# Performance work log

Hardware: AMD Instinct MI355X
Metric: run time of the kernel (lower is better)

## Reference

```python
import jax, jax.numpy as jnp
import numpy as np

B, L, D, W = 4, 256, 256, 8  # batch, seq_len, d_model, context_window
NS_EPS = 1e-7


def setup_inputs() -> dict:
    key = jax.random.key(0)
    ks = jax.random.split(key, 12)
    f = lambda k, s: jax.random.normal(k, s, dtype=jnp.float32)
    sD = 1.0 / np.sqrt(D)
    return {
        "x": f(ks[0], (B, L, D)),
        "k_aligned": jnp.tanh(f(ks[1], (B, L, D))),  # QKProjectionLayer applies tanh upstream
        "v": f(ks[2], (B, L, D)),
        "M_prev": f(ks[3], (B, D, D)) * 0.01,
        "S_prev": jnp.zeros((B, D, D), jnp.float32),
        # polynomial feature coeffs: phi(k) = c1*k + c2*k^2 (degree 2, dim-preserving)
        "poly_coeffs": jnp.stack([jnp.ones((D,), jnp.float32), 0.1 * jnp.ones((D,), jnp.float32)])
        + 0.01 * f(ks[4], (2, D)),
        "alpha_W": f(ks[5], (D, D)) * sD, "alpha_b": jnp.zeros((D,), jnp.float32),
        "eta_W": f(ks[6], (D, D)) * sD, "eta_b": jnp.zeros((D,), jnp.float32),
        "theta_W": f(ks[7], (D, D)) * sD, "theta_b": jnp.zeros((D,), jnp.float32),
        "gamma_W": f(ks[8], (D,)) * sD, "gamma_b": jnp.zeros((1,), jnp.float32),
        "out_W": f(ks[9], (D, D)) * sD, "out_b": jnp.zeros((D,), jnp.float32),
    }


def _newton_schulz_1(S):
    # NS_K with K=1: X <- 1.5*X - 0.5*X X^T X after Frobenius normalization
    norm = jnp.sqrt(jnp.sum(S * S, axis=(-2, -1), keepdims=True)) + NS_EPS
    X = S / norm
    return 1.5 * X - 0.5 * jnp.einsum('bij,bkj,bkl->bil', X, X, X)


def reference(x, k_aligned, v, M_prev, S_prev, poly_coeffs,
              alpha_W, alpha_b, eta_W, eta_b, theta_W, theta_b,
              gamma_W, gamma_b, out_W, out_b):
    Bn, Ln, Dn = x.shape
    # polynomial feature layer (dim-preserving, degree 2)
    k_phi = poly_coeffs[0] * k_aligned + poly_coeffs[1] * k_aligned ** 2  # [B,L,D]
    # per-token gates (precomputed, pure linear+sigmoid)
    alpha = jax.nn.sigmoid(x @ alpha_W.T + alpha_b)          # [B,L,D]
    eta = jax.nn.sigmoid(x @ eta_W.T + eta_b) * 0.1          # [B,L,D]
    theta = jax.nn.sigmoid(x @ theta_W.T + theta_b)          # [B,L,D]
    gamma = jax.nn.sigmoid(jnp.einsum('bld,d->bl', x, gamma_W) + gamma_b[0])  # [B,L]
    c_arr = jnp.minimum(jnp.arange(Ln) + 1, W).astype(x.dtype)  # actual window length per step

    to_t = lambda a: jnp.moveaxis(a, 1, 0)  # [B,L,...] -> [L,B,...]
    xs = (to_t(k_phi), to_t(v), to_t(gamma), to_t(alpha), to_t(eta), to_t(theta), c_arr)

    buf_k = jnp.zeros((Bn, W, Dn), x.dtype)  # sliding window of phi(k); zero pads contribute 0
    buf_v = jnp.zeros((Bn, W, Dn), x.dtype)
    buf_g = jnp.zeros((Bn, W), x.dtype)

    def step(carry, xt):
        M, S, bk, bv, bg = carry
        k_t, v_t, g_t, a_t, e_t, th_t, c_t = xt
        bk = jnp.concatenate([bk[:, 1:], k_t[:, None]], axis=1)
        bv = jnp.concatenate([bv[:, 1:], v_t[:, None]], axis=1)
        bg = jnp.concatenate([bg[:, 1:], g_t[:, None]], axis=1)
        # Omega gradient: sum_i gamma_i * (M phi(k_i) - v_i) outer phi(k_i) / c
        pred = jnp.einsum('bde,bwe->bwd', M, bk)
        err = pred - bv
        grad = jnp.einsum('bw,bwd,bwe->bde', bg, err, bk) / c_t
        S = th_t[..., None] * S + grad
        S_ortho = _newton_schulz_1(S)
        M = a_t[..., None] * M - e_t[..., None] * S_ortho
        y = jnp.einsum('bde,be->bd', M, k_t)
        return (M, S, bk, bv, bg), y

    (M, S, _, _, _), ys = jax.lax.scan(step, (M_prev, S_prev, buf_k, buf_v, buf_g), xs)
    output = jnp.moveaxis(ys, 0, 1) @ out_W.T + out_b  # out_proj per token
    return (output, M, S)
```

## Files before the change

### kernel.cpp

```cpp
#include <hip/hip_runtime.h>

#define Bn 4
#define Ln 256
#define Dn 256
#define Wn 8
#define NBLK 64
#define BLD (Bn*Ln*Dn)
#define BDD (Bn*Dn*Dn)

typedef float  floatx4 __attribute__((ext_vector_type(4)));
typedef short  short8  __attribute__((ext_vector_type(8)));

__device__ __forceinline__ float ldc(const float* p) {
    return __hip_atomic_load(p, __ATOMIC_RELAXED, __HIP_MEMORY_SCOPE_AGENT);
}
__device__ __forceinline__ void stc(float* p, float v) {
    __hip_atomic_store(p, v, __ATOMIC_RELAXED, __HIP_MEMORY_SCOPE_AGENT);
}
__device__ __forceinline__ void stc4(float* p, floatx4 v) {
    asm volatile("global_store_dwordx4 %0, %1, off sc0 sc1" :: "v"(p), "v"(v) : "memory");
}
__device__ __forceinline__ void ldc1x4(float& a, float& b, float& c, float& d,
    const float* p0, const float* p1, const float* p2, const float* p3)
{
    asm volatile(
        "global_load_dword %0, %4, off sc0 sc1\n\t"
        "global_load_dword %1, %5, off sc0 sc1\n\t"
        "global_load_dword %2, %6, off sc0 sc1\n\t"
        "global_load_dword %3, %7, off sc0 sc1\n\t"
        "s_waitcnt vmcnt(0)"
        : "=&v"(a), "=&v"(b), "=&v"(c), "=&v"(d)
        : "v"(p0), "v"(p1), "v"(p2), "v"(p3)
        : "memory");
}
__device__ __forceinline__ void ldc4x12s(
    floatx4& r0, floatx4& r1, floatx4& r2, floatx4& r3,
    floatx4& r4, floatx4& r5, floatx4& r6, floatx4& r7,
    floatx4& r8, floatx4& r9, floatx4& r10, floatx4& r11, float& sc,
    const float* p0, const float* p1, const float* p2, const float* p3,
    const float* p4, const float* p5, const float* p6, const float* p7,
    const float* p8, const float* p9, const float* p10, const float* p11,
    const float* ps)
{
    asm volatile(
        "global_load_dwordx4 %0, %13, off sc0 sc1\n\t"
        "global_load_dwordx4 %1, %14, off sc0 sc1\n\t"
        "global_load_dwordx4 %2, %15, off sc0 sc1\n\t"
        "global_load_dwordx4 %3, %16, off sc0 sc1\n\t"
        "global_load_dwordx4 %4, %17, off sc0 sc1\n\t"
        "global_load_dwordx4 %5, %18, off sc0 sc1\n\t"
        "global_load_dwordx4 %6, %19, off sc0 sc1\n\t"
        "global_load_dwordx4 %7, %20, off sc0 sc1\n\t"
        "global_load_dwordx4 %8, %21, off sc0 sc1\n\t"
        "global_load_dwordx4 %9, %22, off sc0 sc1\n\t"
        "global_load_dwordx4 %10, %23, off sc0 sc1\n\t"
        "global_load_dwordx4 %11, %24, off sc0 sc1\n\t"
        "global_load_dword %12, %25, off sc0 sc1\n\t"
        "s_waitcnt vmcnt(0)"
        : "=&v"(r0), "=&v"(r1), "=&v"(r2), "=&v"(r3),
          "=&v"(r4), "=&v"(r5), "=&v"(r6), "=&v"(r7),
          "=&v"(r8), "=&v"(r9), "=&v"(r10), "=&v"(r11), "=&v"(sc)
        : "v"(p0), "v"(p1), "v"(p2), "v"(p3), "v"(p4), "v"(p5),
          "v"(p6), "v"(p7), "v"(p8), "v"(p9), "v"(p10), "v"(p11), "v"(ps)
        : "memory");
}

__device__ __forceinline__ unsigned f2bf(float x) {
    unsigned u = __float_as_uint(x);
    return (u + 0x7FFFu + ((u >> 16) & 1u)) >> 16;
}
__device__ __forceinline__ unsigned long long packbf4(floatx4 v) {
    unsigned lo = f2bf(v[0]) | (f2bf(v[1]) << 16);
    unsigned hi = f2bf(v[2]) | (f2bf(v[3]) << 16);
    return (unsigned long long)lo | ((unsigned long long)hi << 32);
}
union BF8 { short8 s8; unsigned long long u[2]; };

__device__ __forceinline__ void grid_sync_b(unsigned* bflags, int rem, unsigned k)
// ... 110 lines not shown

__global__ __launch_bounds__(256) void ysum_kernel(float* __restrict__ ysp)
{
    int gidx = blockIdx.x * 256 + threadIdx.x;
    float4 a = ((float4*)ysp)[gidx];
    float4 b = ((float4*)ysp)[65536 + gidx];
    float4 c = ((float4*)ysp)[131072 + gidx];
    float4 d = ((float4*)ysp)[196608 + gidx];
    a.x += b.x + c.x + d.x;
    a.y += b.y + c.y + d.y;
    a.z += b.z + c.z + d.z;
    a.w += b.w + c.w + d.w;
    ((float4*)ysp)[gidx] = a;
}

#define OFF_ST    0
#define OFF_UV    8448
#define OFF_AV    10496
#define OFF_CV    12544
#define OFF_TH    14592
#define OFF_KT    14848
#define OFF_KL    15104
#define OFF_NRM   15168
#define OFF_WSUM  15184
#define OFF_US    15200
#define OFF_KWA   15328
#define OFF_KW2   17408
#define OFF_SL    19456
#define SMEM_FLOATS 23616

__global__ void __launch_bounds__(256, 1) scan_kernel(
    const float* __restrict__ kphi, const float* __restrict__ vin,
    const float* __restrict__ gammaB, const float* __restrict__ alphaB,
    const float* __restrict__ etaB, const float* __restrict__ thetaB,
    const float* __restrict__ Kall,
    const float* __restrict__ Mprev, const float* __restrict__ Sprev,
    unsigned short* __restrict__ STg,
    float* __restrict__ u_buf, float* __restrict__ a_buf,
    float* __restrict__ errp_g, float* __restrict__ normp,
    float* __restrict__ ysp, unsigned* __restrict__ flags,
    float* __restrict__ outM, float* __restrict__ outS)
{
    __shared__ float smem[SMEM_FLOATS];
    char*  STb  = (char*)(smem + OFF_ST);
    float* uvp  = smem + OFF_UV;
    float* avp  = smem + OFF_AV;
    float* cvp  = smem + OFF_CV;
    float* thv  = smem + OFF_TH;
    float* kT   = smem + OFF_KT;
    float* Kl   = smem + OFF_KL;
    float* nrml = smem + OFF_NRM;
    float* wsum = smem + OFF_WSUM;
    float* usl  = smem + OFF_US;
    float* kWA  = smem + OFF_KWA;
    float* kW2  = smem + OFF_KW2;
    float* Sl   = smem + OFF_SL;

    const int wg = blockIdx.x, tid = threadIdx.x;
    const int b   = wg >> 4;
    const int rem = wg & 15;
    const int s   = rem & 3;
    const int i0 = (rem >> 2) * 64, l0 = (rem & 3) * 64;
    const int d0 = rem << 4;
    const int wid = tid >> 6, lane = tid & 63;
    const int lme = lane & 15, hi = lane >> 4;
    const int ibr = i0 + wid * 16 + (hi << 2);
    const int r  = tid >> 4, m = tid & 15;
    unsigned* bflags = flags + b * 512;
    unsigned kbar = 0;

    floatx4 S_reg[4];
    float   M_reg[16];
    floatx4 T_reg[16];

    {
#pragma unroll
        for (int cq = 0; cq < 4; ++cq)
            S_reg[cq] = *(const floatx4*)&Sprev[(size_t)(b*256 + d0 + r)*256 + m*4 + 64*cq];
#pragma unroll
        for (int lt = 0; lt < 4; ++lt)
#pragma unroll
            for (int g = 0; g < 4; ++g)
                M_reg[lt*4+g] = Mprev[(size_t)(b*256 + ibr + g)*256 + l0 + lt*16 + lme];

        float* scratch = smem;
        for (int g4 = 0; g4 < 4; ++g4) {
            floatx4 acc[4];
#pragma unroll
            for (int lt = 0; lt < 4; ++lt) acc[lt] = (floatx4){0.f,0.f,0.f,0.f};
#pragma unroll
            for (int kc = 0; kc < 8; ++kc) {
                int kb2 = kc*32 + hi*8;
                floatx4 a0 = *(const floatx4*)&Sprev[(size_t)(b*256 + i0 + wid*16 + lme)*256 + kb2];
// ... 8 lines not shown
                    acc[lt] = __builtin_amdgcn_mfma_f32_16x16x32_bf16(ua.s8, ub.s8, acc[lt], 0,0,0);
                }
            }
#pragma unroll
            for (int lt = 0; lt < 4; ++lt)
#pragma unroll
                for (int g = 0; g < 4; ++g)
                    scratch[(wid*16 + (hi<<2) + g)*260 + g4*64 + lt*16 + lme] = acc[lt][g];
        }
        __syncthreads();
#pragma unroll
        for (int kc = 0; kc < 8; ++kc) {
            T_reg[kc*2+0] = *(floatx4*)&scratch[(wid*16 + lme)*260 + kc*32 + hi*8];
            T_reg[kc*2+1] = *(floatx4*)&scratch[(wid*16 + lme)*260 + kc*32 + hi*8 + 4];
        }
#pragma unroll
        for (int q = 0; q < 2; ++q) {
            int w = q*4 + (tid >> 6);
            int c4 = (tid & 63) << 2;
            floatx4 kv = {0.f,0.f,0.f,0.f};
            if (w == 7) kv = *(const floatx4*)&kphi[(size_t)(b*Ln)*Dn + c4];
            *(floatx4*)&kW2[w*256 + c4] = kv;
        }
        __syncthreads();
#pragma unroll
        for (int w = 0; w < 8; ++w) {
            float pd[4] = {0.f,0.f,0.f,0.f};
#pragma unroll
            for (int lt = 0; lt < 4; ++lt) {
                float kv2 = kW2[w*256 + l0 + lt*16 + lme];
#pragma unroll
                for (int g = 0; g < 4; ++g) pd[g] += M_reg[lt*4+g] * kv2;
            }
#pragma unroll
            for (int g = 0; g < 4; ++g) {
                pd[g] += __shfl_xor(pd[g], 1); pd[g] += __shfl_xor(pd[g], 2);
                pd[g] += __shfl_xor(pd[g], 4); pd[g] += __shfl_xor(pd[g], 8);
            }
            if (lme == 0)
#pragma unroll
                for (int g = 0; g < 4; ++g)
                    stc(&errp_g[(size_t)((s*2 + 0)*4 + b)*2048 + w*256 + ibr + g], pd[g]);
        }
    }
    grid_sync_b(bflags, rem, ++kbar);

    for (int t = 0; t < Ln; ++t) {
        const int cwin = (t + 1 < Wn) ? (t + 1) : Wn;
        const float invc = 1.f / (float)cwin;

        {
            float e0_ = 0.f, e1_ = 0.f, e2_ = 0.f, e3_ = 0.f;
            int w_a = 0, rr_a = 0;
            const int p = t & 1;
            if (tid < 128) {
                w_a = tid >> 4; rr_a = tid & 15;
                ldc1x4(e0_, e1_, e2_, e3_,
                    &errp_g[(size_t)((0*2 + p)*4 + b)*2048 + w_a*256 + d0 + rr_a],
                    &errp_g[(size_t)((1*2 + p)*4 + b)*2048 + w_a*256 + d0 + rr_a],
                    &errp_g[(size_t)((2*2 + p)*4 + b)*2048 + w_a*256 + d0 + rr_a],
                    &errp_g[(size_t)((3*2 + p)*4 + b)*2048 + w_a*256 + d0 + rr_a]);
                float ep = e0_ + e1_ + e2_ + e3_;
                int tok = t - 7 + w_a;
                float uu = 0.f;
                if (tok >= 0)
                    uu = gammaB[b*Ln + tok] * invc *
                         (ep - vin[(size_t)(b*Ln + tok)*Dn + d0 + rr_a]);
                usl[w_a*16 + rr_a] = uu;
                stc(&u_buf[(size_t)(b*8 + w_a)*256 + d0 + rr_a], uu);
            } else {
                int idx = tid - 128;
                int w = idx >> 4, seg = idx & 15;
                int tk = t - 7 + w;
#pragma unroll
                for (int q = 0; q < 4; ++q) {
                    floatx4 kv = {0.f,0.f,0.f,0.f};
                    if (tk >= 0)
                        kv = *(const floatx4*)&kphi[(size_t)(b*Ln + tk)*Dn + seg*16 + q*4];
                    *(floatx4*)&kWA[w*260 + seg*16 + q*4] = kv;
                }
            }
            __syncthreads();

            {
                float qw[8] = {0,0,0,0,0,0,0,0};
#pragma unroll
                for (int cq = 0; cq < 4; ++cq) {
                    floatx4 sv = S_reg[cq];
#pragma unroll
                    for (int w = 0; w < 8; ++w) {
                        floatx4 kv = *(const floatx4*)&kWA[w*260 + m*4 + 64*cq];
                        qw[w] += sv[0]*kv[0] + sv[1]*kv[1] + sv[2]*kv[2] + sv[3]*kv[3];
                    }
                }
#pragma unroll
                for (int w = 0; w < 8; ++w) {
                    qw[w] += __shfl_xor(qw[w], 1); qw[w] += __shfl_xor(qw[w], 2);
                    qw[w] += __shfl_xor(qw[w], 4); qw[w] += __shfl_xor(qw[w], 8);
                }
                if (m < 8) {
                    float th = thetaB[(size_t)(b*Ln + t)*Dn + d0 + r];
                    stc(&a_buf[(size_t)(b*8 + m)*256 + d0 + r], th * qw[m]);
                }
            }
            {
                float th = thetaB[(size_t)(b*Ln + t)*Dn + d0 + r];
                float uu[8];
#pragma unroll
                for (int w = 0; w < 8; ++w) uu[w] = usl[w*16 + r];
                float sumsq = 0.f;
#pragma unroll
                for (int cq = 0; cq < 4; ++cq) {
                    floatx4 sv = th * S_reg[cq];
#pragma unroll
                    for (int w = 0; w < 8; ++w) {
                        floatx4 kv = *(const floatx4*)&kWA[w*260 + m*4 + 64*cq];
                        sv += uu[w] * kv;
                    }
                    S_reg[cq] = sv;
                    sumsq += sv[0]*sv[0] + sv[1]*sv[1] + sv[2]*sv[2] + sv[3]*sv[3];
                }
#pragma unroll
                for (int off = 32; off; off >>= 1) sumsq += __shfl_xor(sumsq, off);
                if (lane == 0) wsum[wid] = sumsq;
            }
            {
#pragma unroll
                for (int cq = 0; cq < 4; ++cq)
                    *(floatx4*)&Sl[r*260 + m*4 + 64*cq] = S_reg[cq];
                __syncthreads();
                int l = tid;
                unsigned dw[8];
#pragma unroll
                for (int j = 0; j < 8; ++j)
                    dw[j] = f2bf(Sl[(2*j)*260 + l]) | (f2bf(Sl[(2*j+1)*260 + l]) << 16);
                floatx4 p0 = { __uint_as_float(dw[0]), __uint_as_float(dw[1]),
                               __uint_as_float(dw[2]), __uint_as_float(dw[3]) };
                floatx4 p1 = { __uint_as_float(dw[4]), __uint_as_float(dw[5]),
                               __uint_as_float(dw[6]), __uint_as_float(dw[7]) };
                char* dstp = (char*)STg + ((size_t)(b*256 + l)*256 + d0)*2;
                stc4((float*)dstp, p0);
                stc4((float*)(dstp + 16), p1);
                if (tid == 0)
                    stc(&normp[b*16 + rem], wsum[0] + wsum[1] + wsum[2] + wsum[3]);
            }
            if (t == Ln - 1) {
#pragma unroll
                for (int cq = 0; cq < 4; ++cq)
                    *(floatx4*)&outS[(size_t)(b*256 + d0 + r)*256 + m*4 + 64*cq] = S_reg[cq];
            }
        }
        grid_sync_b(bflags, rem, ++kbar);

        {
            {
                int lq = tid >> 2, kq = (tid & 3) * 64;
                const char* src = (const char*)STg + ((size_t)(b*256 + l0 + lq)*256 + kq)*2;
                const float* pu = &u_buf[(size_t)b*2048 + tid*8];
                const float* pa = &a_buf[(size_t)b*2048 + tid*8];
                const float* pn = (tid < 16) ? &normp[b*16 + tid] : pu;
                floatx4 r0,r1,r2,r3,r4,r5,r6,r7,u0,u1,a0,a1; float nsc;
                ldc4x12s(r0,r1,r2,r3,r4,r5,r6,r7,u0,u1,a0,a1,nsc,
                    (const float*)(src+0),  (const float*)(src+16),
                    (const float*)(src+32), (const float*)(src+48),
                    (const float*)(src+64), (const float*)(src+80),
                    (const float*)(src+96), (const float*)(src+112),
                    pu, pu+4, pa, pa+4, pn);
                size_t rb0 = (size_t)lq*528 + (size_t)kq*2;
                unsigned swz = (unsigned)((lq & 8) << 1);
                *(floatx4*)(STb + ((rb0 +   0) ^ swz)) = r0;
                *(floatx4*)(STb + ((rb0 +  16) ^ swz)) = r1;
                *(floatx4*)(STb + ((rb0 +  32) ^ swz)) = r2;
                *(floatx4*)(STb + ((rb0 +  48) ^ swz)) = r3;
                *(floatx4*)(STb + ((rb0 +  64) ^ swz)) = r4;
                *(floatx4*)(STb + ((rb0 +  80) ^ swz)) = r5;
                *(floatx4*)(STb + ((rb0 +  96) ^ swz)) = r6;
                *(floatx4*)(STb + ((rb0 + 112) ^ swz)) = r7;
                *(floatx4*)&uvp[tid*8]     = u0; *(floatx4*)&uvp[tid*8 + 4] = u1;
                *(floatx4*)&avp[tid*8]     = a0; *(floatx4*)&avp[tid*8 + 4] = a1;
                if (tid < 16) nrml[tid] = nsc;
                if (tid < 64) {
                    *(floatx4*)&thv[tid*4] = *(const floatx4*)&thetaB[(size_t)(b*Ln + t)*Dn + tid*4];
                    *(floatx4*)&kT[tid*4]  = *(const floatx4*)&kphi[(size_t)(b*Ln + t)*Dn + tid*4];
                }
                if (tid < 16)
                    *(floatx4*)&Kl[tid*4] = *(const floatx4*)&Kall[(size_t)(b*Ln + t)*64 + tid*4];
                if (t < Ln - 1) {
#pragma unroll
                    for (int q = 0; q < 2; ++q) {
                        int w = q*4 + (tid >> 6);
                        int c4 = (tid & 63) << 2;
                        int tk = t + 1 - 7 + w;
                        floatx4 kv = {0.f,0.f,0.f,0.f};
                        if (tk >= 0) kv = *(const floatx4*)&kphi[(size_t)(b*Ln + tk)*Dn + c4];
                        *(floatx4*)&kW2[w*256 + c4] = kv;
                    }
                }
            }
            __syncthreads();

#pragma unroll
            for (int q = 0; q < 8; ++q) {
                int idx = q*256 + tid;
                int w = idx >> 8, e = idx & 255;
                float sv = avp[idx];
#pragma unroll
                for (int w2 = 0; w2 < 8; ++w2)
                    sv += 0.5f * Kl[w*8 + w2] * uvp[w2*256 + e];
                cvp[idx] = sv;
            }
            __syncthreads();

            {
                int i = i0 + wid*16 + lme;
                float thi = thv[i];
                float ui8[8], ci8[8];
#pragma unroll
                for (int w = 0; w < 8; ++w) { ui8[w] = uvp[w*256 + i]; ci8[w] = cvp[w*256 + i]; }
#pragma unroll
                for (int kc = 0; kc < 8; ++kc) {
                    int k0 = kc*32 + hi*8;
                    floatx4 th0 = *(const floatx4*)&thv[k0];
                    floatx4 th1 = *(const floatx4*)&thv[k0 + 4];
                    floatx4 t0 = (thi * th0) * T_reg[kc*2+0];
                    floatx4 t1 = (thi * th1) * T_reg[kc*2+1];
#pragma unroll
                    for (int w = 0; w < 8; ++w) {
                        floatx4 uk0 = *(const floatx4*)&uvp[w*256 + k0];
                        floatx4 uk1 = *(const floatx4*)&uvp[w*256 + k0 + 4];
                        floatx4 ck0 = *(const floatx4*)&cvp[w*256 + k0];
                        floatx4 ck1 = *(const floatx4*)&cvp[w*256 + k0 + 4];
                        t0 += ui8[w]*ck0 + ci8[w]*uk0;
                        t1 += ui8[w]*ck1 + ci8[w]*uk1;
                    }
                    T_reg[kc*2+0] = t0;
                    T_reg[kc*2+1] = t1;
                }
            }

            floatx4 acc[4];
#pragma unroll
            for (int lt = 0; lt < 4; ++lt) acc[lt] = (floatx4){0.f,0.f,0.f,0.f};
#pragma unroll
            for (int kc = 0; kc < 8; ++kc) {
                BF8 ua; ua.u[0] = packbf4(T_reg[kc*2]); ua.u[1] = packbf4(T_reg[kc*2+1]);
                int kbyte = kc*64 + hi*16;
#pragma unroll
                for (int lt = 0; lt < 4; ++lt) {
                    int row = lt*16 + lme;
                    short8 bf = *(const short8*)(STb +
                        (((size_t)row*528 + kbyte) ^ (unsigned)((row & 8) << 1)));
                    acc[lt] = __builtin_amdgcn_mfma_f32_16x16x32_bf16(ua.s8, bf, acc[lt], 0,0,0);
                }
            }

            {
                float nsq = 0.f;
#pragma unroll
                for (int q = 0; q < 16; ++q) nsq += nrml[q];
                float nrm = sqrtf(nsq) + 1e-7f;
                float inv_n = 1.f / nrm;
                float w1 = 1.5f * inv_n;
                float w3 = 0.5f * inv_n * inv_n * inv_n;
                float alv[4], etv[4], kvr[4];
#pragma unroll
                for (int g = 0; g < 4; ++g) {
                    alv[g] = alphaB[(size_t)(b*Ln + t)*Dn + ibr + g];
                    etv[g] = etaB[(size_t)(b*Ln + t)*Dn + ibr + g];
                }
#pragma unroll
                for (int lt = 0; lt < 4; ++lt) kvr[lt] = kT[l0 + lt*16 + lme];
                float py[4] = {0.f,0.f,0.f,0.f};
#pragma unroll
                for (int lt = 0; lt < 4; ++lt)
#pragma unroll
                    for (int g = 0; g < 4; ++g) {
                        int l_loc = lt*16 + lme;
                        unsigned short sb = *(const unsigned short*)(STb +
                            (((size_t)l_loc*528 + (size_t)(ibr + g)*2) ^ (unsigned)((l_loc & 8) << 1)));
                        float s_il = __uint_as_float(((unsigned)sb) << 16);
                        float ns = w1 * s_il - w3 * acc[lt][g];
                        float mn = alv[g] * M_reg[lt*4+g] - etv[g] * ns;
                        M_reg[lt*4+g] = mn;
                        py[g] += mn * kvr[lt];
                        if (t == Ln - 1)
                            outM[(size_t)(b*256 + ibr + g)*256 + l0 + l_loc] = mn;
                    }
#pragma unroll
                for (int g = 0; g < 4; ++g) {
                    py[g] += __shfl_xor(py[g], 1); py[g] += __shfl_xor(py[g], 2);
                    py[g] += __shfl_xor(py[g], 4); py[g] += __shfl_xor(py[g], 8);
                    if (lme == 0)
                        stc(&ysp[(size_t)s*BLD + (size_t)(b*Ln + t)*Dn + ibr + g], py[g]);
                }
            }

            if (t < Ln - 1) {
                const int p2 = (t + 1) & 1;
#pragma unroll
                for (int w = 0; w < 8; ++w) {
                    float pd[4] = {0.f,0.f,0.f,0.f};
#pragma unroll
                    for (int lt = 0; lt < 4; ++lt) {
                        float kv2 = kW2[w*256 + l0 + lt*16 + lme];
#pragma unroll
                        for (int g = 0; g < 4; ++g) pd[g] += M_reg[lt*4+g] * kv2;
                    }
#pragma unroll
                    for (int g = 0; g < 4; ++g) {
                        pd[g] += __shfl_xor(pd[g], 1); pd[g] += __shfl_xor(pd[g], 2);
                        pd[g] += __shfl_xor(pd[g], 4); pd[g] += __shfl_xor(pd[g], 8);
                    }
                    if (lme == 0)
#pragma unroll
                        for (int g = 0; g < 4; ++g)
                            stc(&errp_g[(size_t)((s*2 + p2)*4 + b)*2048 + w*256 + ibr + g], pd[g]);
                }
            }
        }
        grid_sync_b(bflags, rem, ++kbar);
    }
}

extern "C" void kernel_launch(void* const* d_in, const int* in_sizes, int n_in,
                              void* d_out, int out_size, void* d_ws, size_t ws_size,
                              hipStream_t stream)
{
    const float* x       = (const float*)d_in[0];
    const float* k_al    = (const float*)d_in[1];
    const float* v       = (const float*)d_in[2];
    const float* M_prev  = (const float*)d_in[3];
// ... 5 lines not shown
    const float* eta_b   = (const float*)d_in[9];
    const float* theta_W = (const float*)d_in[10];
    const float* theta_b = (const float*)d_in[11];
    const float* gamma_W = (const float*)d_in[12];
    const float* gamma_b = (const float*)d_in[13];
    const float* out_W   = (const float*)d_in[14];
    const float* out_b   = (const float*)d_in[15];

    float* ws = (float*)d_ws;
    float* kphi    = ws;
    float* alphaB  = kphi   + BLD;
    float* etaB    = alphaB + BLD;
    float* thetaB  = etaB   + BLD;
    float* gammaB  = thetaB + BLD;
    float* Kall    = gammaB + Bn*Ln;
    float* STg_f   = Kall   + Bn*Ln*64;
    float* u_bufp  = STg_f  + 131072;
    float* a_bufp  = u_bufp + Bn*Wn*Dn;
    float* errp    = a_bufp + Bn*Wn*Dn;
    float* normp   = errp   + 65536;
    float* ysp     = normp  + 64;
    unsigned* flags = (unsigned*)(ysp + 4*BLD);

    float* out_y = (float*)d_out;
    float* outM  = out_y + BLD;
    float* outS  = outM + BDD;

    hipLaunchKernelGGL(kphi_gamma_kernel, dim3(256), dim3(256), 0, stream,
                       k_al, x, poly, gamma_W, gamma_b, kphi, gammaB);
    hipLaunchKernelGGL((gemm_act_kernel<1>), dim3(32, 4), dim3(256), 0, stream,
                       x, alpha_W, alpha_b, alphaB);
    hipLaunchKernelGGL((gemm_act_kernel<2>), dim3(32, 4), dim3(256), 0, stream,
                       x, eta_W, eta_b, etaB);
    hipLaunchKernelGGL((gemm_act_kernel<1>), dim3(32, 4), dim3(256), 0, stream,
                       x, theta_W, theta_b, thetaB);
    hipLaunchKernelGGL(kgram_kernel, dim3(Ln, Bn), dim3(64), 0, stream,
                       kphi, Kall);
    hipLaunchKernelGGL(prologue_kernel, dim3(2), dim3(256), 0, stream, flags);

    hipLaunchKernelGGL(scan_kernel, dim3(NBLK), dim3(256), 0, stream,
                       kphi, v, gammaB, alphaB, etaB, thetaB, Kall,
                       M_prev, S_prev, (unsigned short*)STg_f,
                       u_bufp, a_bufp, errp, normp, ysp, flags,
                       outM, outS);

    hipLaunchKernelGGL(ysum_kernel, dim3(256), dim3(256), 0, stream, ysp);
    hipLaunchKernelGGL((gemm_act_kernel<0>), dim3(32, 4), dim3(256), 0, stream,
                       ysp, out_W, out_b, out_y);
}
```

Before: 5.753 ms.

## Keep S column slice resident per block and update Frobenius norm algebraically

Each block now keeps its slice of S (as fp32 columns plus a bf16 transposed copy) in shared memory instead of exchanging S^T and u/a buffers through global memory. The squared row norms of S are carried in registers and updated each step using theta, the cross terms u·(S k) and the window Gram matrix, so no separate norm reduction pass is needed. Partial S·k products (qp) are published alongside the prediction partials and read in one batched coherent load per step. The aim is fewer grid-wide syncs and less global traffic per step. In exchange it uses more shared memory and introduces a recursive norm update that can accumulate rounding drift.

```diff
diff --git a/kernel.cpp b/kernel.cpp
--- a/kernel.cpp
+++ b/kernel.cpp
@@ -11,9 +11,6 @@
 typedef float  floatx4 __attribute__((ext_vector_type(4)));
 typedef short  short8  __attribute__((ext_vector_type(8)));
 
-__device__ __forceinline__ float ldc(const float* p) {
-    return __hip_atomic_load(p, __ATOMIC_RELAXED, __HIP_MEMORY_SCOPE_AGENT);
-}
 __device__ __forceinline__ void stc(float* p, float v) {
     __hip_atomic_store(p, v, __ATOMIC_RELAXED, __HIP_MEMORY_SCOPE_AGENT);
 }
@@ -33,35 +30,38 @@
         : "v"(p0), "v"(p1), "v"(p2), "v"(p3)
         : "memory");
 }
-__device__ __forceinline__ void ldc4x12s(
-    floatx4& r0, floatx4& r1, floatx4& r2, floatx4& r3,
-    floatx4& r4, floatx4& r5, floatx4& r6, floatx4& r7,
-    floatx4& r8, floatx4& r9, floatx4& r10, floatx4& r11, float& sc,
-    const float* p0, const float* p1, const float* p2, const float* p3,
-    const float* p4, const float* p5, const float* p6, const float* p7,
-    const float* p8, const float* p9, const float* p10, const float* p11,
-    const float* ps)
+__device__ __forceinline__ void ldc4x16o(
+    floatx4& e00, floatx4& e01, floatx4& e10, floatx4& e11,
+    floatx4& e20, floatx4& e21, floatx4& e30, floatx4& e31,
+    floatx4& q00, floatx4& q01, floatx4& q10, floatx4& q11,
+    floatx4& q20, floatx4& q21, floatx4& q30, floatx4& q31,
+    const float* pe0, const float* pe1, const float* pe2, const float* pe3,
+    const float* pq0, const float* pq1, const float* pq2, const float* pq3)
 {
     asm volatile(
-        "global_load_dwordx4 %0, %13, off sc0 sc1\n\t"
-        "global_load_dwordx4 %1, %14, off sc0 sc1\n\t"
-        "global_load_dwordx4 %2, %15, off sc0 sc1\n\t"
-        "global_load_dwordx4 %3, %16, off sc0 sc1\n\t"
-        "global_load_dwordx4 %4, %17, off sc0 sc1\n\t"
-        "global_load_dwordx4 %5, %18, off sc0 sc1\n\t"
+        "global_load_dwordx4 %0, %16, off sc0 sc1\n\t"
+        "global_load_dwordx4 %1, %16, off offset:16 sc0 sc1\n\t"
+        "global_load_dwordx4 %2, %17, off sc0 sc1\n\t"
+        "global_load_dwordx4 %3, %17, off offset:16 sc0 sc1\n\t"
+        "global_load_dwordx4 %4, %18, off sc0 sc1\n\t"
+        "global_load_dwordx4 %5, %18, off offset:16 sc0 sc1\n\t"
         "global_load_dwordx4 %6, %19, off sc0 sc1\n\t"
-        "global_load_dwordx4 %7, %20, off sc0 sc1\n\t"
-        "global_load_dwordx4 %8, %21, off sc0 sc1\n\t"
-        "global_load_dwordx4 %9, %22, off sc0 sc1\n\t"
-        "global_load_dwordx4 %10, %23, off sc0 sc1\n\t"
-        "global_load_dwordx4 %11, %24, off sc0 sc1\n\t"
-        "global_load_dword %12, %25, off sc0 sc1\n\t"
+        "global_load_dwordx4 %7, %19, off offset:16 sc0 sc1\n\t"
+        "global_load_dwordx4 %8, %20, off sc0 sc1\n\t"
+        "global_load_dwordx4 %9, %20, off offset:16 sc0 sc1\n\t"
+        "global_load_dwordx4 %10, %21, off sc0 sc1\n\t"
+        "global_load_dwordx4 %11, %21, off offset:16 sc0 sc1\n\t"
+        "global_load_dwordx4 %12, %22, off sc0 sc1\n\t"
+        "global_load_dwordx4 %13, %22, off offset:16 sc0 sc1\n\t"
+        "global_load_dwordx4 %14, %23, off sc0 sc1\n\t"
+        "global_load_dwordx4 %15, %23, off offset:16 sc0 sc1\n\t"
         "s_waitcnt vmcnt(0)"
-        : "=&v"(r0), "=&v"(r1), "=&v"(r2), "=&v"(r3),
-          "=&v"(r4), "=&v"(r5), "=&v"(r6), "=&v"(r7),
-          "=&v"(r8), "=&v"(r9), "=&v"(r10), "=&v"(r11), "=&v"(sc)
-        : "v"(p0), "v"(p1), "v"(p2), "v"(p3), "v"(p4), "v"(p5),
-          "v"(p6), "v"(p7), "v"(p8), "v"(p9), "v"(p10), "v"(p11), "v"(ps)
+        : "=&v"(e00), "=&v"(e01), "=&v"(e10), "=&v"(e11),
+          "=&v"(e20), "=&v"(e21), "=&v"(e30), "=&v"(e31),
+          "=&v"(q00), "=&v"(q01), "=&v"(q10), "=&v"(q11),
+          "=&v"(q20), "=&v"(q21), "=&v"(q30), "=&v"(q31)
+        : "v"(pe0), "v"(pe1), "v"(pe2), "v"(pe3),
+          "v"(pq0), "v"(pq1), "v"(pq2), "v"(pq3)
         : "memory");
 }
 
@@ -202,20 +202,17 @@
     ((float4*)ysp)[gidx] = a;
 }
 
-#define OFF_ST    0
-#define OFF_UV    8448
-#define OFF_AV    10496
-#define OFF_CV    12544
-#define OFF_TH    14592
-#define OFF_KT    14848
-#define OFF_KL    15104
-#define OFF_NRM   15168
-#define OFF_WSUM  15184
-#define OFF_US    15200
-#define OFF_KWA   15328
-#define OFF_KW2   17408
-#define OFF_SL    19456
-#define SMEM_FLOATS 23616
+#define OFF_SCOL 0
+#define OFF_STBF 16640
+#define OFF_UV   25088
+#define OFF_QV   27168
+#define OFF_CV   29248
+#define OFF_TH   31328
+#define OFF_KWA  31584
+#define OFF_KNX  33664
+#define OFF_KL   33924
+#define OFF_RED  33988
+#define SMEM_FLOATS 34000
 
 __global__ void __launch_bounds__(256, 1) scan_kernel(
     const float* __restrict__ kphi, const float* __restrict__ vin,
@@ -223,48 +220,39 @@
     const float* __restrict__ etaB, const float* __restrict__ thetaB,
     const float* __restrict__ Kall,
     const float* __restrict__ Mprev, const float* __restrict__ Sprev,
-    unsigned short* __restrict__ STg,
-    float* __restrict__ u_buf, float* __restrict__ a_buf,
-    float* __restrict__ errp_g, float* __restrict__ normp,
-    float* __restrict__ ysp, unsigned* __restrict__ flags,
+    float* __restrict__ errp, float* __restrict__ qp,
+    float* __restrict__ rsqp, float* __restrict__ ysp,
+    unsigned* __restrict__ flags,
     float* __restrict__ outM, float* __restrict__ outS)
 {
     __shared__ float smem[SMEM_FLOATS];
-    char*  STb  = (char*)(smem + OFF_ST);
-    float* uvp  = smem + OFF_UV;
-    float* avp  = smem + OFF_AV;
-    float* cvp  = smem + OFF_CV;
-    float* thv  = smem + OFF_TH;
-    float* kT   = smem + OFF_KT;
-    float* Kl   = smem + OFF_KL;
-    float* nrml = smem + OFF_NRM;
-    float* wsum = smem + OFF_WSUM;
-    float* usl  = smem + OFF_US;
-    float* kWA  = smem + OFF_KWA;
-    float* kW2  = smem + OFF_KW2;
-    float* Sl   = smem + OFF_SL;
+    float* Scol  = smem + OFF_SCOL;
+    char*  STbB  = (char*)(smem + OFF_STBF);
+    float* uv    = smem + OFF_UV;
+    float* qv    = smem + OFF_QV;
+    float* cv    = smem + OFF_CV;
+    float* thv   = smem + OFF_TH;
+    float* kWA   = smem + OFF_KWA;
+    float* kNext = smem + OFF_KNX;
+    float* Kl    = smem + OFF_KL;
+    float* red   = smem + OFF_RED;
 
     const int wg = blockIdx.x, tid = threadIdx.x;
     const int b   = wg >> 4;
     const int rem = wg & 15;
     const int s   = rem & 3;
     const int i0 = (rem >> 2) * 64, l0 = (rem & 3) * 64;
-    const int d0 = rem << 4;
     const int wid = tid >> 6, lane = tid & 63;
     const int lme = lane & 15, hi = lane >> 4;
     const int ibr = i0 + wid * 16 + (hi << 2);
-    const int r  = tid >> 4, m = tid & 15;
     unsigned* bflags = flags + b * 512;
     unsigned kbar = 0;
 
-    floatx4 S_reg[4];
     float   M_reg[16];
     floatx4 T_reg[16];
+    float   rowsq_r;
 
     {
-#pragma unroll
-        for (int cq = 0; cq < 4; ++cq)
-            S_reg[cq] = *(const floatx4*)&Sprev[(size_t)(b*256 + d0 + r)*256 + m*4 + 64*cq];
 #pragma unroll
         for (int lt = 0; lt < 4; ++lt)
 #pragma unroll
@@ -303,21 +291,46 @@
             T_reg[kc*2+0] = *(floatx4*)&scratch[(wid*16 + lme)*260 + kc*32 + hi*8];
             T_reg[kc*2+1] = *(floatx4*)&scratch[(wid*16 + lme)*260 + kc*32 + hi*8 + 4];
         }
-#pragma unroll
-        for (int q = 0; q < 2; ++q) {
-            int w = q*4 + (tid >> 6);
-            int c4 = (tid & 63) << 2;
-            floatx4 kv = {0.f,0.f,0.f,0.f};
-            if (w == 7) kv = *(const floatx4*)&kphi[(size_t)(b*Ln)*Dn + c4];
-            *(floatx4*)&kW2[w*256 + c4] = kv;
-        }
-        __syncthreads();
+        __syncthreads();
+
+        {
+#pragma unroll
+            for (int c = 0; c < 16; ++c) {
+                floatx4 sv = *(const floatx4*)&Sprev[(size_t)(b*256 + tid)*256 + l0 + c*4];
+#pragma unroll
+                for (int j = 0; j < 4; ++j) {
+                    int e = c*4 + j;
+                    Scol[e*260 + tid] = sv[j];
+                    *(unsigned short*)(STbB +
+                        (((size_t)e*528 + 2*(size_t)tid) ^ (unsigned)((e&8)<<1))) =
+                        (unsigned short)f2bf(sv[j]);
+                }
+            }
+        }
+        {
+#pragma unroll
+            for (int qq = 0; qq < 2; ++qq) {
+                int idx = qq*256 + tid;
+                int w = idx >> 6, c4 = (idx & 63) * 4;
+                floatx4 kv = {0,0,0,0};
+                int tk = 0 - 7 + w;
+                if (tk >= 0) kv = *(const floatx4*)&kphi[(size_t)(b*Ln + tk)*Dn + c4];
+                *(floatx4*)&kWA[w*260 + c4] = kv;
+            }
+        }
+        __syncthreads();
+
+        if ((rem >> 2) == 0) {
+            float sq = 0.f;
+            for (int e = 0; e < 64; ++e) { float sv = Scol[e*260 + tid]; sq += sv*sv; }
+            stc(&rsqp[(s*Bn + b)*256 + tid], sq);
+        }
 #pragma unroll
         for (int w = 0; w < 8; ++w) {
             float pd[4] = {0.f,0.f,0.f,0.f};
 #pragma unroll
             for (int lt = 0; lt < 4; ++lt) {
-                float kv2 = kW2[w*256 + l0 + lt*16 + lme];
+                float kv2 = kWA[w*260 + l0 + lt*16 + lme];
 #pragma unroll
                 for (int g = 0; g < 4; ++g) pd[g] += M_reg[lt*4+g] * kv2;
             }
@@ -326,207 +339,176 @@
                 pd[g] += __shfl_xor(pd[g], 1); pd[g] += __shfl_xor(pd[g], 2);
                 pd[g] += __shfl_xor(pd[g], 4); pd[g] += __shfl_xor(pd[g], 8);
             }
-            if (lme == 0)
-#pragma unroll
-                for (int g = 0; g < 4; ++g)
-                    stc(&errp_g[(size_t)((s*2 + 0)*4 + b)*2048 + w*256 + ibr + g], pd[g]);
-        }
-    }
-    grid_sync_b(bflags, rem, ++kbar);
+            if (lme == 0) {
+                floatx4 pv = {pd[0], pd[1], pd[2], pd[3]};
+                stc4(&errp[(size_t)((s*2 + 0)*4 + b)*2048 + w*256 + ibr], pv);
+            }
+        }
+        {
+            int dq = i0 + (tid >> 2), eq0 = (tid & 3) * 16;
+            float qpd[8] = {0,0,0,0,0,0,0,0};
+            for (int j = 0; j < 16; ++j) {
+                float sv = Scol[(eq0 + j)*260 + dq];
+#pragma unroll
+                for (int w = 0; w < 8; ++w) qpd[w] += sv * kWA[w*260 + l0 + eq0 + j];
+            }
+#pragma unroll
+            for (int w = 0; w < 8; ++w) {
+                qpd[w] += __shfl_xor(qpd[w], 1); qpd[w] += __shfl_xor(qpd[w], 2);
+            }
+            if ((tid & 3) == 0)
+#pragma unroll
+                for (int w = 0; w < 8; ++w)
+                    stc(&qp[(size_t)((s*2 + 0)*4 + b)*2048 + w*256 + dq], qpd[w]);
+        }
+        grid_sync_b(bflags, rem, ++kbar);
+        {
+            float r0, r1, r2, r3;
+            ldc1x4(r0, r1, r2, r3,
+                   &rsqp[(0*Bn + b)*256 + tid], &rsqp[(1*Bn + b)*256 + tid],
+                   &rsqp[(2*Bn + b)*256 + tid], &rsqp[(3*Bn + b)*256 + tid]);
+            rowsq_r = r0 + r1 + r2 + r3;
+        }
+    }
 
     for (int t = 0; t < Ln; ++t) {
         const int cwin = (t + 1 < Wn) ? (t + 1) : Wn;
         const float invc = 1.f / (float)cwin;
-
-        {
-            float e0_ = 0.f, e1_ = 0.f, e2_ = 0.f, e3_ = 0.f;
-            int w_a = 0, rr_a = 0;
-            const int p = t & 1;
-            if (tid < 128) {
-                w_a = tid >> 4; rr_a = tid & 15;
-                ldc1x4(e0_, e1_, e2_, e3_,
-                    &errp_g[(size_t)((0*2 + p)*4 + b)*2048 + w_a*256 + d0 + rr_a],
-                    &errp_g[(size_t)((1*2 + p)*4 + b)*2048 + w_a*256 + d0 + rr_a],
-                    &errp_g[(size_t)((2*2 + p)*4 + b)*2048 + w_a*256 + d0 + rr_a],
-                    &errp_g[(size_t)((3*2 + p)*4 + b)*2048 + w_a*256 + d0 + rr_a]);
-                float ep = e0_ + e1_ + e2_ + e3_;
-                int tok = t - 7 + w_a;
-                float uu = 0.f;
-                if (tok >= 0)
-                    uu = gammaB[b*Ln + tok] * invc *
-                         (ep - vin[(size_t)(b*Ln + tok)*Dn + d0 + rr_a]);
-                usl[w_a*16 + rr_a] = uu;
-                stc(&u_buf[(size_t)(b*8 + w_a)*256 + d0 + rr_a], uu);
-            } else {
-                int idx = tid - 128;
-                int w = idx >> 4, seg = idx & 15;
+        const int p = t & 1;
+
+        {
+#pragma unroll
+            for (int qq = 0; qq < 2; ++qq) {
+                int idx = qq*256 + tid;
+                int w = idx >> 6, c4 = (idx & 63) * 4;
+                floatx4 kv = {0,0,0,0};
                 int tk = t - 7 + w;
-#pragma unroll
-                for (int q = 0; q < 4; ++q) {
-                    floatx4 kv = {0.f,0.f,0.f,0.f};
-                    if (tk >= 0)
-                        kv = *(const floatx4*)&kphi[(size_t)(b*Ln + tk)*Dn + seg*16 + q*4];
-                    *(floatx4*)&kWA[w*260 + seg*16 + q*4] = kv;
-                }
-            }
-            __syncthreads();
-
-            {
-                float qw[8] = {0,0,0,0,0,0,0,0};
-#pragma unroll
-                for (int cq = 0; cq < 4; ++cq) {
-                    floatx4 sv = S_reg[cq];
-#pragma unroll
-                    for (int w = 0; w < 8; ++w) {
-                        floatx4 kv = *(const floatx4*)&kWA[w*260 + m*4 + 64*cq];
-                        qw[w] += sv[0]*kv[0] + sv[1]*kv[1] + sv[2]*kv[2] + sv[3]*kv[3];
-                    }
-                }
+                if (tk >= 0) kv = *(const floatx4*)&kphi[(size_t)(b*Ln + tk)*Dn + c4];
+                *(floatx4*)&kWA[w*260 + c4] = kv;
+            }
+            if (tid < 64) {
+                floatx4 kv = {0,0,0,0};
+                if (t + 1 < Ln) kv = *(const floatx4*)&kphi[(size_t)(b*Ln + t + 1)*Dn + tid*4];
+                *(floatx4*)&kNext[tid*4] = kv;
+                *(floatx4*)&thv[tid*4] = *(const floatx4*)&thetaB[(size_t)(b*Ln + t)*Dn + tid*4];
+            }
+            if (tid < 16)
+                *(floatx4*)&Kl[tid*4] = *(const floatx4*)&Kall[(size_t)(b*Ln + t)*64 + tid*4];
+        }
+        {
+            const int wX = tid >> 5;
+            const int dX = (tid & 31) * 8;
+            const float* pe0 = errp + (size_t)((0*2 + p)*4 + b)*2048 + wX*256 + dX;
+            const float* pe1 = errp + (size_t)((1*2 + p)*4 + b)*2048 + wX*256 + dX;
+            const float* pe2 = errp + (size_t)((2*2 + p)*4 + b)*2048 + wX*256 + dX;
+            const float* pe3 = errp + (size_t)((3*2 + p)*4 + b)*2048 + wX*256 + dX;
+            const float* pq0 = qp   + (size_t)((0*2 + p)*4 + b)*2048 + wX*256 + dX;
+            const float* pq1 = qp   + (size_t)((1*2 + p)*4 + b)*2048 + wX*256 + dX;
+            const float* pq2 = qp   + (size_t)((2*2 + p)*4 + b)*2048 + wX*256 + dX;
+            const float* pq3 = qp   + (size_t)((3*2 + p)*4 + b)*2048 + wX*256 + dX;
+            floatx4 e00,e01,e10,e11,e20,e21,e30,e31;
+            floatx4 q00,q01,q10,q11,q20,q21,q30,q31;
+            ldc4x16o(e00,e01,e10,e11,e20,e21,e30,e31,
+                     q00,q01,q10,q11,q20,q21,q30,q31,
+                     pe0,pe1,pe2,pe3,pq0,pq1,pq2,pq3);
+            floatx4 es0 = e00+e10+e20+e30, es1 = e01+e11+e21+e31;
+            floatx4 qs0 = q00+q10+q20+q30, qs1 = q01+q11+q21+q31;
+            int tok = t - 7 + wX;
+            float ga = 0.f;
+            floatx4 vv0 = {0,0,0,0}, vv1 = {0,0,0,0};
+            if (tok >= 0) {
+                ga = gammaB[b*Ln + tok] * invc;
+                vv0 = *(const floatx4*)&vin[(size_t)(b*Ln + tok)*Dn + dX];
+                vv1 = *(const floatx4*)&vin[(size_t)(b*Ln + tok)*Dn + dX + 4];
+            }
+            floatx4 u0 = ga*(es0 - vv0), u1 = ga*(es1 - vv1);
+            *(floatx4*)&uv[wX*260 + dX]     = u0;
+            *(floatx4*)&uv[wX*260 + dX + 4] = u1;
+            *(floatx4*)&qv[wX*260 + dX]     = qs0;
+            *(floatx4*)&qv[wX*260 + dX + 4] = qs1;
+        }
+        __syncthreads();
+
+        {
+#pragma unroll
+            for (int qq = 0; qq < 8; ++qq) {
+                int idx = qq*256 + tid;
+                int w = idx >> 8, e = idx & 255;
+                float sv = thv[e] * qv[w*260 + e];
+#pragma unroll
+                for (int w2 = 0; w2 < 8; ++w2)
+                    sv += 0.5f * Kl[w*8 + w2] * uv[w2*260 + e];
+                cv[w*260 + e] = sv;
+            }
+            float uu8[8], qq8[8];
+#pragma unroll
+            for (int w = 0; w < 8; ++w) { uu8[w] = uv[w*260 + tid]; qq8[w] = qv[w*260 + tid]; }
+            float th_d = thv[tid];
+            float cross = 0.f, quad = 0.f;
+#pragma unroll
+            for (int w = 0; w < 8; ++w) {
+                cross += uu8[w] * qq8[w];
+                float kk = 0.f;
+#pragma unroll
+                for (int w2 = 0; w2 < 8; ++w2) kk += Kl[w*8 + w2] * uu8[w2];
+                quad += uu8[w] * kk;
+            }
+            float rq = th_d*th_d*rowsq_r + 2.f*th_d*cross + quad;
+            rowsq_r = rq;
+#pragma unroll
+            for (int off = 32; off; off >>= 1) rq += __shfl_xor(rq, off);
+            if (lane == 0) red[wid] = rq;
+        }
+        __syncthreads();
+
+        {
+            int e = tid >> 2, d0s = (tid & 3) * 64;
+            float kv8[8];
+#pragma unroll
+            for (int w = 0; w < 8; ++w) kv8[w] = kWA[w*260 + l0 + e];
+#pragma unroll
+            for (int c = 0; c < 16; ++c) {
+                floatx4 sv = *(floatx4*)&Scol[e*260 + d0s + c*4];
+                floatx4 tv = *(const floatx4*)&thv[d0s + c*4];
+                sv = tv * sv;
 #pragma unroll
                 for (int w = 0; w < 8; ++w) {
-                    qw[w] += __shfl_xor(qw[w], 1); qw[w] += __shfl_xor(qw[w], 2);
-                    qw[w] += __shfl_xor(qw[w], 4); qw[w] += __shfl_xor(qw[w], 8);
-                }
-                if (m < 8) {
-                    float th = thetaB[(size_t)(b*Ln + t)*Dn + d0 + r];
-                    stc(&a_buf[(size_t)(b*8 + m)*256 + d0 + r], th * qw[m]);
-                }
-            }
-            {
-                float th = thetaB[(size_t)(b*Ln + t)*Dn + d0 + r];
-                float uu[8];
-#pragma unroll
-                for (int w = 0; w < 8; ++w) uu[w] = usl[w*16 + r];
-                float sumsq = 0.f;
-#pragma unroll
-                for (int cq = 0; cq < 4; ++cq) {
-                    floatx4 sv = th * S_reg[cq];
-#pragma unroll
-                    for (int w = 0; w < 8; ++w) {
-                        floatx4 kv = *(const floatx4*)&kWA[w*260 + m*4 + 64*cq];
-                        sv += uu[w] * kv;
-                    }
-                    S_reg[cq] = sv;
-                    sumsq += sv[0]*sv[0] + sv[1]*sv[1] + sv[2]*sv[2] + sv[3]*sv[3];
-                }
-#pragma unroll
-                for (int off = 32; off; off >>= 1) sumsq += __shfl_xor(sumsq, off);
-                if (lane == 0) wsum[wid] = sumsq;
-            }
-            {
-#pragma unroll
-                for (int cq = 0; cq < 4; ++cq)
-                    *(floatx4*)&Sl[r*260 + m*4 + 64*cq] = S_reg[cq];
-                __syncthreads();
-                int l = tid;
-                unsigned dw[8];
-#pragma unroll
-                for (int j = 0; j < 8; ++j)
-                    dw[j] = f2bf(Sl[(2*j)*260 + l]) | (f2bf(Sl[(2*j+1)*260 + l]) << 16);
-                floatx4 p0 = { __uint_as_float(dw[0]), __uint_as_float(dw[1]),
-                               __uint_as_float(dw[2]), __uint_as_float(dw[3]) };
-                floatx4 p1 = { __uint_as_float(dw[4]), __uint_as_float(dw[5]),
-                               __uint_as_float(dw[6]), __uint_as_float(dw[7]) };
-                char* dstp = (char*)STg + ((size_t)(b*256 + l)*256 + d0)*2;
-                stc4((float*)dstp, p0);
-                stc4((float*)(dstp + 16), p1);
-                if (tid == 0)
-                    stc(&normp[b*16 + rem], wsum[0] + wsum[1] + wsum[2] + wsum[3]);
-            }
-            if (t == Ln - 1) {
-#pragma unroll
-                for (int cq = 0; cq < 4; ++cq)
-                    *(floatx4*)&outS[(size_t)(b*256 + d0 + r)*256 + m*4 + 64*cq] = S_reg[cq];
-            }
-        }
-        grid_sync_b(bflags, rem, ++kbar);
-
-        {
-            {
-                int lq = tid >> 2, kq = (tid & 3) * 64;
-                const char* src = (const char*)STg + ((size_t)(b*256 + l0 + lq)*256 + kq)*2;
-                const float* pu = &u_buf[(size_t)b*2048 + tid*8];
-                const float* pa = &a_buf[(size_t)b*2048 + tid*8];
-                const float* pn = (tid < 16) ? &normp[b*16 + tid] : pu;
-                floatx4 r0,r1,r2,r3,r4,r5,r6,r7,u0,u1,a0,a1; float nsc;
-                ldc4x12s(r0,r1,r2,r3,r4,r5,r6,r7,u0,u1,a0,a1,nsc,
-                    (const float*)(src+0),  (const float*)(src+16),
-                    (const float*)(src+32), (const float*)(src+48),
-                    (const float*)(src+64), (const float*)(src+80),
-                    (const float*)(src+96), (const float*)(src+112),
-                    pu, pu+4, pa, pa+4, pn);
-                size_t rb0 = (size_t)lq*528 + (size_t)kq*2;
-                unsigned swz = (unsigned)((lq & 8) << 1);
-                *(floatx4*)(STb + ((rb0 +   0) ^ swz)) = r0;
-                *(floatx4*)(STb + ((rb0 +  16) ^ swz)) = r1;
-                *(floatx4*)(STb + ((rb0 +  32) ^ swz)) = r2;
-                *(floatx4*)(STb + ((rb0 +  48) ^ swz)) = r3;
-                *(floatx4*)(STb + ((rb0 +  64) ^ swz)) = r4;
-                *(floatx4*)(STb + ((rb0 +  80) ^ swz)) = r5;
-                *(floatx4*)(STb + ((rb0 +  96) ^ swz)) = r6;
-                *(floatx4*)(STb + ((rb0 + 112) ^ swz)) = r7;
-                *(floatx4*)&uvp[tid*8]     = u0; *(floatx4*)&uvp[tid*8 + 4] = u1;
-                *(floatx4*)&avp[tid*8]     = a0; *(floatx4*)&avp[tid*8 + 4] = a1;
-                if (tid < 16) nrml[tid] = nsc;
-                if (tid < 64) {
-                    *(floatx4*)&thv[tid*4] = *(const floatx4*)&thetaB[(size_t)(b*Ln + t)*Dn + tid*4];
-                    *(floatx4*)&kT[tid*4]  = *(const floatx4*)&kphi[(size_t)(b*Ln + t)*Dn + tid*4];
-                }
-                if (tid < 16)
-                    *(floatx4*)&Kl[tid*4] = *(const floatx4*)&Kall[(size_t)(b*Ln + t)*64 + tid*4];
-                if (t < Ln - 1) {
-#pragma unroll
-                    for (int q = 0; q < 2; ++q) {
-                        int w = q*4 + (tid >> 6);
-                        int c4 = (tid & 63) << 2;
-                        int tk = t + 1 - 7 + w;
-                        floatx4 kv = {0.f,0.f,0.f,0.f};
-                        if (tk >= 0) kv = *(const floatx4*)&kphi[(size_t)(b*Ln + tk)*Dn + c4];
-                        *(floatx4*)&kW2[w*256 + c4] = kv;
-                    }
-                }
-            }
-            __syncthreads();
-
-#pragma unroll
-            for (int q = 0; q < 8; ++q) {
-                int idx = q*256 + tid;
-                int w = idx >> 8, e = idx & 255;
-                float sv = avp[idx];
-#pragma unroll
-                for (int w2 = 0; w2 < 8; ++w2)
-                    sv += 0.5f * Kl[w*8 + w2] * uvp[w2*256 + e];
-                cvp[idx] = sv;
-            }
-            __syncthreads();
-
-            {
-                int i = i0 + wid*16 + lme;
-                float thi = thv[i];
-                float ui8[8], ci8[8];
-#pragma unroll
-                for (int w = 0; w < 8; ++w) { ui8[w] = uvp[w*256 + i]; ci8[w] = cvp[w*256 + i]; }
-#pragma unroll
-                for (int kc = 0; kc < 8; ++kc) {
-                    int k0 = kc*32 + hi*8;
-                    floatx4 th0 = *(const floatx4*)&thv[k0];
-                    floatx4 th1 = *(const floatx4*)&thv[k0 + 4];
-                    floatx4 t0 = (thi * th0) * T_reg[kc*2+0];
-                    floatx4 t1 = (thi * th1) * T_reg[kc*2+1];
-#pragma unroll
-                    for (int w = 0; w < 8; ++w) {
-                        floatx4 uk0 = *(const floatx4*)&uvp[w*256 + k0];
-                        floatx4 uk1 = *(const floatx4*)&uvp[w*256 + k0 + 4];
-                        floatx4 ck0 = *(const floatx4*)&cvp[w*256 + k0];
-                        floatx4 ck1 = *(const floatx4*)&cvp[w*256 + k0 + 4];
-                        t0 += ui8[w]*ck0 + ci8[w]*uk0;
-                        t1 += ui8[w]*ck1 + ci8[w]*uk1;
-                    }
-                    T_reg[kc*2+0] = t0;
-                    T_reg[kc*2+1] = t1;
-                }
-            }
-
+                    floatx4 uvv = *(const floatx4*)&uv[w*260 + d0s + c*4];
+                    sv += kv8[w] * uvv;
+                }
+                *(floatx4*)&Scol[e*260 + d0s + c*4] = sv;
+                unsigned long long pk = packbf4(sv);
+                *(unsigned long long*)(STbB +
+                    (((size_t)e*528 + 2*(size_t)(d0s + c*4)) ^ (unsigned)((e&8)<<1))) = pk;
+            }
+            int i = i0 + wid*16 + lme;
+            float thi = thv[i];
+            float ui8[8], ci8[8];
+#pragma unroll
+            for (int w = 0; w < 8; ++w) { ui8[w] = uv[w*260 + i]; ci8[w] = cv[w*260 + i]; }
+#pragma unroll
+            for (int kc = 0; kc < 8; ++kc) {
+                int k0 = kc*32 + hi*8;
+                floatx4 th0 = *(const floatx4*)&thv[k0];
+                floatx4 th1 = *(const floatx4*)&thv[k0 + 4];
+                floatx4 t0 = (thi * th0) * T_reg[kc*2+0];
+                floatx4 t1 = (thi * th1) * T_reg[kc*2+1];
+#pragma unroll
+                for (int w = 0; w < 8; ++w) {
+                    floatx4 uk0 = *(const floatx4*)&uv[w*260 + k0];
+                    floatx4 uk1 = *(const floatx4*)&uv[w*260 + k0 + 4];
+                    floatx4 ck0 = *(const floatx4*)&cv[w*260 + k0];
+                    floatx4 ck1 = *(const floatx4*)&cv[w*260 + k0 + 4];
+                    t0 += ui8[w]*ck0 + ci8[w]*uk0;
+                    t1 += ui8[w]*ck1 + ci8[w]*uk1;
+                }
+                T_reg[kc*2+0] = t0;
+                T_reg[kc*2+1] = t1;
+            }
+        }
+        __syncthreads();
+
+        {
             floatx4 acc[4];
 #pragma unroll
             for (int lt = 0; lt < 4; ++lt) acc[lt] = (floatx4){0.f,0.f,0.f,0.f};
@@ -537,73 +519,97 @@
 #pragma unroll
                 for (int lt = 0; lt < 4; ++lt) {
                     int row = lt*16 + lme;
-                    short8 bf = *(const short8*)(STb +
+                    short8 bf = *(const short8*)(STbB +
                         (((size_t)row*528 + kbyte) ^ (unsigned)((row & 8) << 1)));
                     acc[lt] = __builtin_amdgcn_mfma_f32_16x16x32_bf16(ua.s8, bf, acc[lt], 0,0,0);
                 }
             }
-
+            float nsq = red[0] + red[1] + red[2] + red[3];
+            float nrm = sqrtf(nsq) + 1e-7f;
+            float inv_n = 1.f / nrm;
+            float w1 = 1.5f * inv_n;
+            float w3 = 0.5f * inv_n * inv_n * inv_n;
+            float alv[4], etv[4], kvr[4];
+#pragma unroll
+            for (int g = 0; g < 4; ++g) {
+                alv[g] = alphaB[(size_t)(b*Ln + t)*Dn + ibr + g];
+                etv[g] = etaB[(size_t)(b*Ln + t)*Dn + ibr + g];
+            }
+#pragma unroll
+            for (int lt = 0; lt < 4; ++lt) kvr[lt] = kWA[7*260 + l0 + lt*16 + lme];
+            float py[4] = {0.f,0.f,0.f,0.f};
+#pragma unroll
+            for (int lt = 0; lt < 4; ++lt)
+#pragma unroll
+                for (int g = 0; g < 4; ++g) {
+                    int l_loc = lt*16 + lme;
+                    float s_il = Scol[l_loc*260 + ibr + g];
+                    float ns = w1 * s_il - w3 * acc[lt][g];
+                    float mn = alv[g] * M_reg[lt*4+g] - etv[g] * ns;
+                    M_reg[lt*4+g] = mn;
+                    py[g] += mn * kvr[lt];
+                    if (t == Ln - 1)
+                        outM[(size_t)(b*256 + ibr + g)*256 + l0 + l_loc] = mn;
+                }
+#pragma unroll
+            for (int g = 0; g < 4; ++g) {
+                py[g] += __shfl_xor(py[g], 1); py[g] += __shfl_xor(py[g], 2);
+                py[g] += __shfl_xor(py[g], 4); py[g] += __shfl_xor(py[g], 8);
+                if (lme == 0)
+                    stc(&ysp[(size_t)s*BLD + (size_t)(b*Ln + t)*Dn + ibr + g], py[g]);
+            }
+        }
+
+        if (t < Ln - 1) {
+            const int p2 = (t + 1) & 1;
+#pragma unroll
+            for (int w = 0; w < 8; ++w) {
+                float pd[4] = {0.f,0.f,0.f,0.f};
+#pragma unroll
+                for (int lt = 0; lt < 4; ++lt) {
+                    int li = l0 + lt*16 + lme;
+                    float kv2 = (w < 7) ? kWA[(w+1)*260 + li] : kNext[li];
+#pragma unroll
+                    for (int g = 0; g < 4; ++g) pd[g] += M_reg[lt*4+g] * kv2;
+                }
+#pragma unroll
+                for (int g = 0; g < 4; ++g) {
+                    pd[g] += __shfl_xor(pd[g], 1); pd[g] += __shfl_xor(pd[g], 2);
+                    pd[g] += __shfl_xor(pd[g], 4); pd[g] += __shfl_xor(pd[g], 8);
+                }
+                if (lme == 0) {
+                    floatx4 pv = {pd[0], pd[1], pd[2], pd[3]};
+                    stc4(&errp[(size_t)((s*2 + p2)*4 + b)*2048 + w*256 + ibr], pv);
+                }
+            }
             {
-                float nsq = 0.f;
-#pragma unroll
-                for (int q = 0; q < 16; ++q) nsq += nrml[q];
-                float nrm = sqrtf(nsq) + 1e-7f;
-                float inv_n = 1.f / nrm;
-                float w1 = 1.5f * inv_n;
-                float w3 = 0.5f * inv_n * inv_n * inv_n;
-                float alv[4], etv[4], kvr[4];
-#pragma unroll
-                for (int g = 0; g < 4; ++g) {
-                    alv[g] = alphaB[(size_t)(b*Ln + t)*Dn + ibr + g];
-                    etv[g] = etaB[(size_t)(b*Ln + t)*Dn + ibr + g];
-                }
-#pragma unroll
-                for (int lt = 0; lt < 4; ++lt) kvr[lt] = kT[l0 + lt*16 + lme];
-                float py[4] = {0.f,0.f,0.f,0.f};
-#pragma unroll
-                for (int lt = 0; lt < 4; ++lt)
-#pragma unroll
-                    for (int g = 0; g < 4; ++g) {
-                        int l_loc = lt*16 + lme;
-                        unsigned short sb = *(const unsigned short*)(STb +
-                            (((size_t)l_loc*528 + (size_t)(ibr + g)*2) ^ (unsigned)((l_loc & 8) << 1)));
-                        float s_il = __uint_as_float(((unsigned)sb) << 16);
-                        float ns = w1 * s_il - w3 * acc[lt][g];
-                        float mn = alv[g] * M_reg[lt*4+g] - etv[g] * ns;
-                        M_reg[lt*4+g] = mn;
-                        py[g] += mn * kvr[lt];
-                        if (t == Ln - 1)
-                            outM[(size_t)(b*256 + ibr + g)*256 + l0 + l_loc] = mn;
-                    }
-#pragma unroll
-                for (int g = 0; g < 4; ++g) {
-                    py[g] += __shfl_xor(py[g], 1); py[g] += __shfl_xor(py[g], 2);
-                    py[g] += __shfl_xor(py[g], 4); py[g] += __shfl_xor(py[g], 8);
-                    if (lme == 0)
-                        stc(&ysp[(size_t)s*BLD + (size_t)(b*Ln + t)*Dn + ibr + g], py[g]);
-                }
-            }
-
-            if (t < Ln - 1) {
-                const int p2 = (t + 1) & 1;
+                int dq = i0 + (tid >> 2), eq0 = (tid & 3) * 16;
+                float qpd[8] = {0,0,0,0,0,0,0,0};
+                for (int j = 0; j < 16; ++j) {
+                    int li = l0 + eq0 + j;
+                    float sv = Scol[(eq0 + j)*260 + dq];
+#pragma unroll
+                    for (int w = 0; w < 8; ++w)
+                        qpd[w] += sv * ((w < 7) ? kWA[(w+1)*260 + li] : kNext[li]);
+                }
 #pragma unroll
                 for (int w = 0; w < 8; ++w) {
-                    float pd[4] = {0.f,0.f,0.f,0.f};
-#pragma unroll
-                    for (int lt = 0; lt < 4; ++lt) {
-                        float kv2 = kW2[w*256 + l0 + lt*16 + lme];
-#pragma unroll
-                        for (int g = 0; g < 4; ++g) pd[g] += M_reg[lt*4+g] * kv2;
-                    }
-#pragma unroll
-                    for (int g = 0; g < 4; ++g) {
-                        pd[g] += __shfl_xor(pd[g], 1); pd[g] += __shfl_xor(pd[g], 2);
-                        pd[g] += __shfl_xor(pd[g], 4); pd[g] += __shfl_xor(pd[g], 8);
-                    }
-                    if (lme == 0)
-#pragma unroll
-                        for (int g = 0; g < 4; ++g)
-                            stc(&errp_g[(size_t)((s*2 + p2)*4 + b)*2048 + w*256 + ibr + g], pd[g]);
+                    qpd[w] += __shfl_xor(qpd[w], 1); qpd[w] += __shfl_xor(qpd[w], 2);
+                }
+                if ((tid & 3) == 0)
+#pragma unroll
+                    for (int w = 0; w < 8; ++w)
+                        stc(&qp[(size_t)((s*2 + p2)*4 + b)*2048 + w*256 + dq], qpd[w]);
+            }
+        } else if ((rem >> 2) == 0) {
+            for (int c = 0; c < 4; ++c) {
+                float tb_[16];
+#pragma unroll
+                for (int j = 0; j < 16; ++j) tb_[j] = Scol[(c*16 + j)*260 + tid];
+#pragma unroll
+                for (int g2 = 0; g2 < 4; ++g2) {
+                    floatx4 ov = {tb_[g2*4], tb_[g2*4+1], tb_[g2*4+2], tb_[g2*4+3]};
+                    *(floatx4*)&outS[(size_t)(b*256 + tid)*256 + l0 + c*16 + g2*4] = ov;
                 }
             }
         }
@@ -639,12 +645,10 @@
     float* thetaB  = etaB   + BLD;
     float* gammaB  = thetaB + BLD;
     float* Kall    = gammaB + Bn*Ln;
-    float* STg_f   = Kall   + Bn*Ln*64;
-    float* u_bufp  = STg_f  + 131072;
-    float* a_bufp  = u_bufp + Bn*Wn*Dn;
-    float* errp    = a_bufp + Bn*Wn*Dn;
-    float* normp   = errp   + 65536;
-    float* ysp     = normp  + 64;
+    float* errp    = Kall   + Bn*Ln*64;
+    float* qp      = errp   + 65536;
+    float* rsqp    = qp     + 65536;
+    float* ysp     = rsqp   + 4096;
     unsigned* flags = (unsigned*)(ysp + 4*BLD);
 
     float* out_y = (float*)d_out;
@@ -665,8 +669,7 @@
 
     hipLaunchKernelGGL(scan_kernel, dim3(NBLK), dim3(256), 0, stream,
                        kphi, v, gammaB, alphaB, etaB, thetaB, Kall,
-                       M_prev, S_prev, (unsigned short*)STg_f,
-                       u_bufp, a_bufp, errp, normp, ysp, flags,
+                       M_prev, S_prev, errp, qp, rsqp, ysp, flags,
                        outM, outS);
 
     hipLaunchKernelGGL(ysum_kernel, dim3(256), dim3(256), 0, stream, ysp);
```

Measured after the change: 8.532 ms. +48.3%, slower.
